# Performance work log

Measured on AMD Instinct MI355X. Metric: run time of the kernel, lower is better.

The kernel has to match this reference:

```python
import jax, jax.numpy as jnp
import numpy as np

N_NODES = 50000
DEG = 16
N_EDGES = N_NODES * DEG  # 800000
C_IN = 64
C_OUT = 64


def setup_inputs() -> dict:
    key = jax.random.key(0)
    k_x, k_src, k_ea, k_w, k_b = jax.random.split(key, 5)
    x = jax.random.normal(k_x, (N_NODES, C_IN), dtype=jnp.float32)
    # Every node appears DEG times as a destination -> no empty segments in max-aggregation.
    dst = jnp.repeat(jnp.arange(N_NODES, dtype=jnp.int32), DEG)
    src = jax.random.randint(k_src, (N_EDGES,), 0, N_NODES, dtype=jnp.int32)
    edge_index = jnp.stack([src, dst], axis=0)  # [2, E], row0=source(j), row1=target(i)
    edge_attr = jax.random.normal(k_ea, (N_EDGES, 1), dtype=jnp.float32)  # unused by forward (faithful to source)
    # MLP(2*C_IN -> C_OUT): Linear weight [out, 2*in] + bias, kaiming-ish scale
    W = jax.random.normal(k_w, (C_OUT, 2 * C_IN), dtype=jnp.float32) * (1.0 / np.sqrt(2 * C_IN))
    b = jax.random.normal(k_b, (C_OUT,), dtype=jnp.float32) * 0.01
    return {"x": x, "edge_index": edge_index, "edge_attr": edge_attr, "W": W, "b": b}


def reference(x, edge_index, edge_attr, W, b):
    # PyG EdgeConv: out_i = max_{j in N(i)} MLP(concat(x_i, x_j - x_i)); aggr='max'
    src = edge_index[0]  # j (source)
    dst = edge_index[1]  # i (target)
    x_i = x[dst]                      # [E, C]
    x_j = x[src]                      # [E, C]
    feat = jnp.concatenate([x_i, x_j - x_i], axis=-1)   # [E, 2C]
    msg = jax.nn.relu(feat @ W.T + b)                    # [E, C_out] per-edge MLP
    out = jax.ops.segment_max(msg, dst, num_segments=x.shape[0])  # scatter-max
    # Guard against -inf for isolated nodes (none by construction, but match scatter fill=0)
    return jnp.where(jnp.isneginf(out), 0.0, out)
```

## Files before the change

### kernel.cpp

```cpp
#include <hip/hip_runtime.h>


#define DEG 16
#define C 64
#define NPW 16
#define WPB 4

typedef __attribute__((ext_vector_type(8))) short s16x8;
typedef __attribute__((ext_vector_type(4))) float f32x4;

__device__ __forceinline__ unsigned short f2bf(float f) {
    union { float f; unsigned u; } v; v.f = f;
    unsigned u = v.u + 0x7FFFu + ((v.u >> 16) & 1u);
    return (unsigned short)(u >> 16);
}

__global__ __launch_bounds__(256) void cvt_bf16(const float* __restrict__ x,
                                                unsigned short* __restrict__ xb,
                                                int n4) {
    int i = blockIdx.x * blockDim.x + threadIdx.x;
    if (i >= n4) return;
    f32x4 v = ((const f32x4*)x)[i];
    ushort4 o;
    o.x = f2bf(v[0]); o.y = f2bf(v[1]); o.z = f2bf(v[2]); o.w = f2bf(v[3]);
    ((ushort4*)xb)[i] = o;
}

template<bool PRE>
__device__ __forceinline__ s16x8 load_frag(const float* __restrict__ x,
                                           const unsigned short* __restrict__ xb,
                                           int row, int koff) {
    if constexpr (PRE) {
        return *(const s16x8*)(xb + row * C + koff);
    } else {
        const float* p = x + row * C + koff;
        f32x4 a = *(const f32x4*)p;
        f32x4 b = *(const f32x4*)(p + 4);
        s16x8 r;
        r[0] = (short)f2bf(a[0]); r[1] = (short)f2bf(a[1]);
        r[2] = (short)f2bf(a[2]); r[3] = (short)f2bf(a[3]);
        r[4] = (short)f2bf(b[0]); r[5] = (short)f2bf(b[1]);
        r[6] = (short)f2bf(b[2]); r[7] = (short)f2bf(b[3]);
        return r;
    }
}

template<bool PRE>
__global__ __launch_bounds__(256, 2) void edgeconv_mfma(
    const float* __restrict__ x,
    const unsigned short* __restrict__ xb,
    const int* __restrict__ src,
    const float* __restrict__ W,
    const float* __restrict__ bias,
    float* __restrict__ out,
    int n_groups)
{
    const int lane = threadIdx.x & 63;
    const int wave = threadIdx.x >> 6;
    const int col  = lane & 15;
    const int quad = lane >> 4;
    int group = blockIdx.x * WPB + wave;
    if (group >= n_groups) group = n_groups - 1;

    s16x8 b2[4][2];
    f32x4 baseD[4];
    {
        s16x8 bd[4][2];
        #pragma unroll
        for (int nt = 0; nt < 4; ++nt) {
            const float* wrow = W + (nt * 16 + col) * (2 * C);
            #pragma unroll
            for (int ks = 0; ks < 2; ++ks) {
                const int k0 = ks * 32 + quad * 8;
                f32x4 w1a = *(const f32x4*)(wrow + k0);
                f32x4 w1b = *(const f32x4*)(wrow + k0 + 4);
                f32x4 w2a = *(const f32x4*)(wrow + C + k0);
                f32x4 w2b = *(const f32x4*)(wrow + C + k0 + 4);
                s16x8 t2, td;
                #pragma unroll
                for (int j = 0; j < 4; ++j) {
                    t2[j]     = (short)f2bf(w2a[j]);
                    t2[j + 4] = (short)f2bf(w2b[j]);
                    td[j]     = (short)f2bf(w1a[j] - w2a[j]);
                    td[j + 4] = (short)f2bf(w1b[j] - w2b[j]);
                }
                b2[nt][ks] = t2;
                bd[nt][ks] = td;
            }
        }
        #pragma unroll
        for (int nt = 0; nt < 4; ++nt) {
            float bv = bias[nt * 16 + col];
            baseD[nt] = (f32x4){bv, bv, bv, bv};
        }
        const int nrow = group * NPW + col;
        s16x8 xi0 = load_frag<PRE>(x, xb, nrow, quad * 8);
        s16x8 xi1 = load_frag<PRE>(x, xb, nrow, 32 + quad * 8);
        #pragma unroll
        for (int nt = 0; nt < 4; ++nt) {
            baseD[nt] = __builtin_amdgcn_mfma_f32_16x16x32_bf16(xi0, bd[nt][0], baseD[nt], 0, 0, 0);
            baseD[nt] = __builtin_amdgcn_mfma_f32_16x16x32_bf16(xi1, bd[nt][1], baseD[nt], 0, 0, 0);
        }
    }

    int idx[NPW];
    #pragma unroll
    for (int n = 0; n < NPW; ++n)
        idx[n] = src[group * (NPW * DEG) + n * DEG + col];

    s16x8 xa[3][2];
    #pragma unroll
    for (int p = 0; p < 2; ++p) {
        xa[p][0] = load_frag<PRE>(x, xb, idx[p], quad * 8);
        xa[p][1] = load_frag<PRE>(x, xb, idx[p], 32 + quad * 8);
    }

    #pragma unroll
    for (int n = 0; n < NPW; ++n) {
        if (n + 2 < NPW) {
            xa[(n + 2) % 3][0] = load_frag<PRE>(x, xb, idx[n + 2], quad * 8);
            xa[(n + 2) % 3][1] = load_frag<PRE>(x, xb, idx[n + 2], 32 + quad * 8);
        }
        const int slane = ((n >> 2) << 4) | col;
        f32x4 acc[4];
        #pragma unroll
        for (int nt = 0; nt < 4; ++nt) {
            float bb = __shfl(baseD[nt][n & 3], slane);
            acc[nt] = (f32x4){bb, bb, bb, bb};
        }
        #pragma unroll
        for (int nt = 0; nt < 4; ++nt) {
            acc[nt] = __builtin_amdgcn_mfma_f32_16x16x32_bf16(xa[n % 3][0], b2[nt][0], acc[nt], 0, 0, 0);
            acc[nt] = __builtin_amdgcn_mfma_f32_16x16x32_bf16(xa[n % 3][1], b2[nt][1], acc[nt], 0, 0, 0);
        }
        float m[4];
        #pragma unroll
        for (int nt = 0; nt < 4; ++nt) {
            float t = fmaxf(fmaxf(acc[nt][0], acc[nt][1]),
                            fmaxf(acc[nt][2], acc[nt][3]));
            t = fmaxf(t, __shfl_xor(t, 16));
            t = fmaxf(t, __shfl_xor(t, 32));
            m[nt] = t;
        }
        float r = quad == 0 ? m[0] : quad == 1 ? m[1] : quad == 2 ? m[2] : m[3];
        r = fmaxf(r, 0.0f);
        out[(group * NPW + n) * C + lane] = r;
    }
}

extern "C" void kernel_launch(void* const* d_in, const int* in_sizes, int n_in,
                              void* d_out, int out_size, void* d_ws, size_t ws_size,
                              hipStream_t stream) {
    const float* x    = (const float*)d_in[0];
    const int*   src  = (const int*)  d_in[1];
    const float* W    = (const float*)d_in[3];
    const float* b    = (const float*)d_in[4];
    float*       out  = (float*)d_out;

    const int n_nodes  = in_sizes[0] / C;
    const int n_groups = (n_nodes + NPW - 1) / NPW;
    const int grid     = (n_groups + WPB - 1) / WPB;

    const size_t need = (size_t)n_nodes * C * sizeof(unsigned short);
    if (ws_size >= need) {
        unsigned short* xbuf = (unsigned short*)d_ws;
        const int n4 = n_nodes * C / 4;
        cvt_bf16<<<(n4 + 255) / 256, 256, 0, stream>>>(x, xbuf, n4);
        edgeconv_mfma<true><<<grid, 256, 0, stream>>>(x, xbuf, src, W, b, out, n_groups);
    } else {
        edgeconv_mfma<false><<<grid, 256, 0, stream>>>(x, nullptr, src, W, b, out, n_groups);
    }
}
```

Baseline: 109.7 us.

## Precompute bf16 weight fragments once and shrink per-wave node group to four

```diff
diff --git a/kernel.cpp b/kernel.cpp
--- a/kernel.cpp
+++ b/kernel.cpp
@@ -3,7 +3,7 @@
 
 #define DEG 16
 #define C 64
-#define NPW 16
+#define NPW 4
 #define WPB 4
 
 typedef __attribute__((ext_vector_type(8))) short s16x8;
@@ -15,57 +15,21 @@
     return (unsigned short)(u >> 16);
 }
 
-__global__ __launch_bounds__(256) void cvt_bf16(const float* __restrict__ x,
-                                                unsigned short* __restrict__ xb,
-                                                int n4) {
+
+__global__ __launch_bounds__(256) void prep(const float* __restrict__ x,
+                                            const float* __restrict__ W,
+                                            unsigned short* __restrict__ ws_u,
+                                            int n4) {
     int i = blockIdx.x * blockDim.x + threadIdx.x;
-    if (i >= n4) return;
-    f32x4 v = ((const f32x4*)x)[i];
-    ushort4 o;
-    o.x = f2bf(v[0]); o.y = f2bf(v[1]); o.z = f2bf(v[2]); o.w = f2bf(v[3]);
-    ((ushort4*)xb)[i] = o;
-}
-
-template<bool PRE>
-__device__ __forceinline__ s16x8 load_frag(const float* __restrict__ x,
-                                           const unsigned short* __restrict__ xb,
-                                           int row, int koff) {
-    if constexpr (PRE) {
-        return *(const s16x8*)(xb + row * C + koff);
-    } else {
-        const float* p = x + row * C + koff;
-        f32x4 a = *(const f32x4*)p;
-        f32x4 b = *(const f32x4*)(p + 4);
-        s16x8 r;
-        r[0] = (short)f2bf(a[0]); r[1] = (short)f2bf(a[1]);
-        r[2] = (short)f2bf(a[2]); r[3] = (short)f2bf(a[3]);
-        r[4] = (short)f2bf(b[0]); r[5] = (short)f2bf(b[1]);
-        r[6] = (short)f2bf(b[2]); r[7] = (short)f2bf(b[3]);
-        return r;
-    }
-}
-
-template<bool PRE>
-__global__ __launch_bounds__(256, 2) void edgeconv_mfma(
-    const float* __restrict__ x,
-    const unsigned short* __restrict__ xb,
-    const int* __restrict__ src,
-    const float* __restrict__ W,
-    const float* __restrict__ bias,
-    float* __restrict__ out,
-    int n_groups)
-{
-    const int lane = threadIdx.x & 63;
-    const int wave = threadIdx.x >> 6;
-    const int col  = lane & 15;
-    const int quad = lane >> 4;
-    int group = blockIdx.x * WPB + wave;
-    if (group >= n_groups) group = n_groups - 1;
-
-    s16x8 b2[4][2];
-    f32x4 baseD[4];
-    {
-        s16x8 bd[4][2];
+    if (i < n4) {
+        f32x4 v = ((const f32x4*)x)[i];
+        ushort4 o;
+        o.x = f2bf(v[0]); o.y = f2bf(v[1]); o.z = f2bf(v[2]); o.w = f2bf(v[3]);
+        ((ushort4*)ws_u)[i] = o;
+    }
+    if (blockIdx.x == 0 && threadIdx.x < 64) {
+        const int lane = threadIdx.x, col = lane & 15, quad = lane >> 4;
+        unsigned short* wf = ws_u + (size_t)n4 * 4;
         #pragma unroll
         for (int nt = 0; nt < 4; ++nt) {
             const float* wrow = W + (nt * 16 + col) * (2 * C);
@@ -84,54 +48,77 @@
                     td[j]     = (short)f2bf(w1a[j] - w2a[j]);
                     td[j + 4] = (short)f2bf(w1b[j] - w2b[j]);
                 }
-                b2[nt][ks] = t2;
-                bd[nt][ks] = td;
+                *(s16x8*)(wf + (((0 * 8) + nt * 2 + ks) * 64 + lane) * 8) = td;
+                *(s16x8*)(wf + (((1 * 8) + nt * 2 + ks) * 64 + lane) * 8) = t2;
             }
         }
-        #pragma unroll
-        for (int nt = 0; nt < 4; ++nt) {
-            float bv = bias[nt * 16 + col];
-            baseD[nt] = (f32x4){bv, bv, bv, bv};
-        }
-        const int nrow = group * NPW + col;
-        s16x8 xi0 = load_frag<PRE>(x, xb, nrow, quad * 8);
-        s16x8 xi1 = load_frag<PRE>(x, xb, nrow, 32 + quad * 8);
-        #pragma unroll
-        for (int nt = 0; nt < 4; ++nt) {
-            baseD[nt] = __builtin_amdgcn_mfma_f32_16x16x32_bf16(xi0, bd[nt][0], baseD[nt], 0, 0, 0);
-            baseD[nt] = __builtin_amdgcn_mfma_f32_16x16x32_bf16(xi1, bd[nt][1], baseD[nt], 0, 0, 0);
-        }
-    }
+    }
+}
+
+__global__ __launch_bounds__(256, 4) void edgeconv_mfma(
+    const unsigned short* __restrict__ xb,
+    const int* __restrict__ src,
+    const float* __restrict__ bias,
+    float* __restrict__ out,
+    int n_groups, int n_nodes)
+{
+    const int lane = threadIdx.x & 63;
+    const int wave = threadIdx.x >> 6;
+    const int col  = lane & 15;
+    const int quad = lane >> 4;
+    int group = blockIdx.x * WPB + wave;
+    if (group >= n_groups) group = n_groups - 1;
+    const int node0 = group * NPW;
 
     int idx[NPW];
     #pragma unroll
     for (int n = 0; n < NPW; ++n)
-        idx[n] = src[group * (NPW * DEG) + n * DEG + col];
-
-    s16x8 xa[3][2];
-    #pragma unroll
-    for (int p = 0; p < 2; ++p) {
-        xa[p][0] = load_frag<PRE>(x, xb, idx[p], quad * 8);
-        xa[p][1] = load_frag<PRE>(x, xb, idx[p], 32 + quad * 8);
-    }
-
+        idx[n] = src[node0 * DEG + n * DEG + col];
+
+    const unsigned short* wf = xb + (size_t)n_nodes * C;
+    s16x8 bd[4][2], b2[4][2];
+    #pragma unroll
+    for (int nt = 0; nt < 4; ++nt)
+        #pragma unroll
+        for (int ks = 0; ks < 2; ++ks) {
+            bd[nt][ks] = *(const s16x8*)(wf + ((nt * 2 + ks) * 64 + lane) * 8);
+            b2[nt][ks] = *(const s16x8*)(wf + ((8 + nt * 2 + ks) * 64 + lane) * 8);
+        }
+
+    const int xirow = node0 + (col & 3);
+    s16x8 xi0 = *(const s16x8*)(xb + xirow * C + quad * 8);
+    s16x8 xi1 = *(const s16x8*)(xb + xirow * C + 32 + quad * 8);
+    f32x4 baseD[4];
+    #pragma unroll
+    for (int nt = 0; nt < 4; ++nt) {
+        float bv = bias[nt * 16 + col];
+        baseD[nt] = (f32x4){bv, bv, bv, bv};
+    }
+    #pragma unroll
+    for (int nt = 0; nt < 4; ++nt) {
+        baseD[nt] = __builtin_amdgcn_mfma_f32_16x16x32_bf16(xi0, bd[nt][0], baseD[nt], 0, 0, 0);
+        baseD[nt] = __builtin_amdgcn_mfma_f32_16x16x32_bf16(xi1, bd[nt][1], baseD[nt], 0, 0, 0);
+    }
+
+    s16x8 xa[NPW][2];
     #pragma unroll
     for (int n = 0; n < NPW; ++n) {
-        if (n + 2 < NPW) {
-            xa[(n + 2) % 3][0] = load_frag<PRE>(x, xb, idx[n + 2], quad * 8);
-            xa[(n + 2) % 3][1] = load_frag<PRE>(x, xb, idx[n + 2], 32 + quad * 8);
-        }
-        const int slane = ((n >> 2) << 4) | col;
+        xa[n][0] = *(const s16x8*)(xb + idx[n] * C + quad * 8);
+        xa[n][1] = *(const s16x8*)(xb + idx[n] * C + 32 + quad * 8);
+    }
+
+    #pragma unroll
+    for (int n = 0; n < NPW; ++n) {
         f32x4 acc[4];
         #pragma unroll
         for (int nt = 0; nt < 4; ++nt) {
-            float bb = __shfl(baseD[nt][n & 3], slane);
+            float bb = __shfl(baseD[nt][n], col);
             acc[nt] = (f32x4){bb, bb, bb, bb};
         }
         #pragma unroll
         for (int nt = 0; nt < 4; ++nt) {
-            acc[nt] = __builtin_amdgcn_mfma_f32_16x16x32_bf16(xa[n % 3][0], b2[nt][0], acc[nt], 0, 0, 0);
-            acc[nt] = __builtin_amdgcn_mfma_f32_16x16x32_bf16(xa[n % 3][1], b2[nt][1], acc[nt], 0, 0, 0);
+            acc[nt] = __builtin_amdgcn_mfma_f32_16x16x32_bf16(xa[n][0], b2[nt][0], acc[nt], 0, 0, 0);
+            acc[nt] = __builtin_amdgcn_mfma_f32_16x16x32_bf16(xa[n][1], b2[nt][1], acc[nt], 0, 0, 0);
         }
         float m[4];
         #pragma unroll
@@ -144,7 +131,105 @@
         }
         float r = quad == 0 ? m[0] : quad == 1 ? m[1] : quad == 2 ? m[2] : m[3];
         r = fmaxf(r, 0.0f);
-        out[(group * NPW + n) * C + lane] = r;
+        out[(node0 + n) * C + lane] = r;
+    }
+}
+
+__global__ __launch_bounds__(256, 2) void edgeconv_fallback(
+    const float* __restrict__ x, const int* __restrict__ src,
+    const float* __restrict__ W, const float* __restrict__ bias,
+    float* __restrict__ out, int n_groups)
+{
+    const int lane = threadIdx.x & 63, wave = threadIdx.x >> 6;
+    const int col = lane & 15, quad = lane >> 4;
+    int group = blockIdx.x * WPB + wave;
+    if (group >= n_groups) group = n_groups - 1;
+
+    auto frag = [&](int row, int koff) {
+        const float* p = x + row * C + koff;
+        f32x4 a = *(const f32x4*)p, b = *(const f32x4*)(p + 4);
+        s16x8 r;
+        #pragma unroll
+        for (int j = 0; j < 4; ++j) {
+            r[j] = (short)f2bf(a[j]); r[j + 4] = (short)f2bf(b[j]);
+        }
+        return r;
+    };
+
+    s16x8 b2[4][2];
+    f32x4 baseD[4];
+    {
+        s16x8 bd[4][2];
+        #pragma unroll
+        for (int nt = 0; nt < 4; ++nt) {
+            const float* wrow = W + (nt * 16 + col) * (2 * C);
+            #pragma unroll
+            for (int ks = 0; ks < 2; ++ks) {
+                const int k0 = ks * 32 + quad * 8;
+                f32x4 w1a = *(const f32x4*)(wrow + k0);
+                f32x4 w1b = *(const f32x4*)(wrow + k0 + 4);
+                f32x4 w2a = *(const f32x4*)(wrow + C + k0);
+                f32x4 w2b = *(const f32x4*)(wrow + C + k0 + 4);
+                s16x8 t2, td;
+                #pragma unroll
+                for (int j = 0; j < 4; ++j) {
+                    t2[j] = (short)f2bf(w2a[j]); t2[j + 4] = (short)f2bf(w2b[j]);
+                    td[j] = (short)f2bf(w1a[j] - w2a[j]);
+                    td[j + 4] = (short)f2bf(w1b[j] - w2b[j]);
+                }
+                b2[nt][ks] = t2; bd[nt][ks] = td;
+            }
+        }
+        #pragma unroll
+        for (int nt = 0; nt < 4; ++nt) {
+            float bv = bias[nt * 16 + col];
+            baseD[nt] = (f32x4){bv, bv, bv, bv};
+        }
+        const int nrow = group * 16 + col;
+        s16x8 xi0 = frag(nrow, quad * 8), xi1 = frag(nrow, 32 + quad * 8);
+        #pragma unroll
+        for (int nt = 0; nt < 4; ++nt) {
+            baseD[nt] = __builtin_amdgcn_mfma_f32_16x16x32_bf16(xi0, bd[nt][0], baseD[nt], 0, 0, 0);
+            baseD[nt] = __builtin_amdgcn_mfma_f32_16x16x32_bf16(xi1, bd[nt][1], baseD[nt], 0, 0, 0);
+        }
+    }
+    int idx[16];
+    #pragma unroll
+    for (int n = 0; n < 16; ++n) idx[n] = src[group * 256 + n * DEG + col];
+    s16x8 xa[3][2];
+    #pragma unroll
+    for (int p = 0; p < 2; ++p) {
+        xa[p][0] = frag(idx[p], quad * 8); xa[p][1] = frag(idx[p], 32 + quad * 8);
+    }
+    #pragma unroll
+    for (int n = 0; n < 16; ++n) {
+        if (n + 2 < 16) {
+            xa[(n + 2) % 3][0] = frag(idx[n + 2], quad * 8);
+            xa[(n + 2) % 3][1] = frag(idx[n + 2], 32 + quad * 8);
+        }
+        const int slane = ((n >> 2) << 4) | col;
+        f32x4 acc[4];
+        #pragma unroll
+        for (int nt = 0; nt < 4; ++nt) {
+            float bb = __shfl(baseD[nt][n & 3], slane);
+            acc[nt] = (f32x4){bb, bb, bb, bb};
+        }
+        #pragma unroll
+        for (int nt = 0; nt < 4; ++nt) {
+            acc[nt] = __builtin_amdgcn_mfma_f32_16x16x32_bf16(xa[n % 3][0], b2[nt][0], acc[nt], 0, 0, 0);
+            acc[nt] = __builtin_amdgcn_mfma_f32_16x16x32_bf16(xa[n % 3][1], b2[nt][1], acc[nt], 0, 0, 0);
+        }
+        float m[4];
+        #pragma unroll
+        for (int nt = 0; nt < 4; ++nt) {
+            float t = fmaxf(fmaxf(acc[nt][0], acc[nt][1]),
+                            fmaxf(acc[nt][2], acc[nt][3]));
+            t = fmaxf(t, __shfl_xor(t, 16));
+            t = fmaxf(t, __shfl_xor(t, 32));
+            m[nt] = t;
+        }
+        float r = quad == 0 ? m[0] : quad == 1 ? m[1] : quad == 2 ? m[2] : m[3];
+        out[(group * 16 + n) * C + lane] = fmaxf(r, 0.0f);
     }
 }
 
@@ -157,17 +242,19 @@
     const float* b    = (const float*)d_in[4];
     float*       out  = (float*)d_out;
 
-    const int n_nodes  = in_sizes[0] / C;
-    const int n_groups = (n_nodes + NPW - 1) / NPW;
-    const int grid     = (n_groups + WPB - 1) / WPB;
-
-    const size_t need = (size_t)n_nodes * C * sizeof(unsigned short);
+    const int n_nodes = in_sizes[0] / C;
+    const size_t need = ((size_t)n_nodes * C + 16 * 64 * 8) * sizeof(unsigned short);
+
     if (ws_size >= need) {
-        unsigned short* xbuf = (unsigned short*)d_ws;
+        unsigned short* ws_u = (unsigned short*)d_ws;
         const int n4 = n_nodes * C / 4;
-        cvt_bf16<<<(n4 + 255) / 256, 256, 0, stream>>>(x, xbuf, n4);
-        edgeconv_mfma<true><<<grid, 256, 0, stream>>>(x, xbuf, src, W, b, out, n_groups);
+        const int n_groups = (n_nodes + NPW - 1) / NPW;
+        const int grid = (n_groups + WPB - 1) / WPB;
+        prep<<<(n4 + 255) / 256, 256, 0, stream>>>(x, W, ws_u, n4);
+        edgeconv_mfma<<<grid, 256, 0, stream>>>(ws_u, src, b, out, n_groups, n_nodes);
     } else {
-        edgeconv_mfma<false><<<grid, 256, 0, stream>>>(x, nullptr, src, W, b, out, n_groups);
-    }
-}
+        const int n_groups = (n_nodes + 15) / 16;
+        edgeconv_fallback<<<(n_groups + WPB - 1) / WPB, 256, 0, stream>>>(
+            x, src, W, b, out, n_groups);
+    }
+}
```

Result: faster. 100.1 us (-8.8%).

## Fuse bf16 conversion into gather, halve nodes per wave, deepen prefetch

Applied to the files above, without the earlier changes.

```diff
diff --git a/kernel.cpp b/kernel.cpp
--- a/kernel.cpp
+++ b/kernel.cpp
@@ -1,58 +1,44 @@
 #include <hip/hip_runtime.h>
+#include <hip/hip_bf16.h>
 
 
 #define DEG 16
 #define C 64
-#define NPW 16
+#define NPW 8
 #define WPB 4
+#define PIPE 4
 
 typedef __attribute__((ext_vector_type(8))) short s16x8;
 typedef __attribute__((ext_vector_type(4))) float f32x4;
 
-__device__ __forceinline__ unsigned short f2bf(float f) {
-    union { float f; unsigned u; } v; v.f = f;
-    unsigned u = v.u + 0x7FFFu + ((v.u >> 16) & 1u);
-    return (unsigned short)(u >> 16);
+__device__ __forceinline__ unsigned pk2(float lo, float hi) {
+    __hip_bfloat162 h = __float22bfloat162_rn(make_float2(lo, hi));
+    union { __hip_bfloat162 h; unsigned u; } c; c.h = h;
+    return c.u;
 }
 
-__global__ __launch_bounds__(256) void cvt_bf16(const float* __restrict__ x,
-                                                unsigned short* __restrict__ xb,
-                                                int n4) {
-    int i = blockIdx.x * blockDim.x + threadIdx.x;
-    if (i >= n4) return;
-    f32x4 v = ((const f32x4*)x)[i];
-    ushort4 o;
-    o.x = f2bf(v[0]); o.y = f2bf(v[1]); o.z = f2bf(v[2]); o.w = f2bf(v[3]);
-    ((ushort4*)xb)[i] = o;
+__device__ __forceinline__ s16x8 cvt_frag(f32x4 a, f32x4 b) {
+    union { unsigned u[4]; s16x8 v; } r;
+    r.u[0] = pk2(a[0], a[1]); r.u[1] = pk2(a[2], a[3]);
+    r.u[2] = pk2(b[0], b[1]); r.u[3] = pk2(b[2], b[3]);
+    return r.v;
 }
 
-template<bool PRE>
-__device__ __forceinline__ s16x8 load_frag(const float* __restrict__ x,
-                                           const unsigned short* __restrict__ xb,
-                                           int row, int koff) {
-    if constexpr (PRE) {
-        return *(const s16x8*)(xb + row * C + koff);
-    } else {
-        const float* p = x + row * C + koff;
-        f32x4 a = *(const f32x4*)p;
-        f32x4 b = *(const f32x4*)(p + 4);
-        s16x8 r;
-        r[0] = (short)f2bf(a[0]); r[1] = (short)f2bf(a[1]);
-        r[2] = (short)f2bf(a[2]); r[3] = (short)f2bf(a[3]);
-        r[4] = (short)f2bf(b[0]); r[5] = (short)f2bf(b[1]);
-        r[6] = (short)f2bf(b[2]); r[7] = (short)f2bf(b[3]);
-        return r;
-    }
+__device__ __forceinline__ void load4(f32x4* d, const float* __restrict__ x,
+                                      int row, int quad) {
+    const float* p = x + row * C + quad * 8;
+    d[0] = *(const f32x4*)p;
+    d[1] = *(const f32x4*)(p + 4);
+    d[2] = *(const f32x4*)(p + 32);
+    d[3] = *(const f32x4*)(p + 36);
 }
 
-template<bool PRE>
-__global__ __launch_bounds__(256, 2) void edgeconv_mfma(
+__global__ __launch_bounds__(256, 3) void edgeconv_fused(
     const float* __restrict__ x,
-    const unsigned short* __restrict__ xb,
-    const int* __restrict__ src,
+    const int*   __restrict__ src,
     const float* __restrict__ W,
     const float* __restrict__ bias,
-    float* __restrict__ out,
+    float*       __restrict__ out,
     int n_groups)
 {
     const int lane = threadIdx.x & 63;
@@ -61,66 +47,60 @@
     const int quad = lane >> 4;
     int group = blockIdx.x * WPB + wave;
     if (group >= n_groups) group = n_groups - 1;
-
-    s16x8 b2[4][2];
-    f32x4 baseD[4];
-    {
-        s16x8 bd[4][2];
-        #pragma unroll
-        for (int nt = 0; nt < 4; ++nt) {
-            const float* wrow = W + (nt * 16 + col) * (2 * C);
-            #pragma unroll
-            for (int ks = 0; ks < 2; ++ks) {
-                const int k0 = ks * 32 + quad * 8;
-                f32x4 w1a = *(const f32x4*)(wrow + k0);
-                f32x4 w1b = *(const f32x4*)(wrow + k0 + 4);
-                f32x4 w2a = *(const f32x4*)(wrow + C + k0);
-                f32x4 w2b = *(const f32x4*)(wrow + C + k0 + 4);
-                s16x8 t2, td;
-                #pragma unroll
-                for (int j = 0; j < 4; ++j) {
-                    t2[j]     = (short)f2bf(w2a[j]);
-                    t2[j + 4] = (short)f2bf(w2b[j]);
-                    td[j]     = (short)f2bf(w1a[j] - w2a[j]);
-                    td[j + 4] = (short)f2bf(w1b[j] - w2b[j]);
-                }
-                b2[nt][ks] = t2;
-                bd[nt][ks] = td;
-            }
-        }
-        #pragma unroll
-        for (int nt = 0; nt < 4; ++nt) {
-            float bv = bias[nt * 16 + col];
-            baseD[nt] = (f32x4){bv, bv, bv, bv};
-        }
-        const int nrow = group * NPW + col;
-        s16x8 xi0 = load_frag<PRE>(x, xb, nrow, quad * 8);
-        s16x8 xi1 = load_frag<PRE>(x, xb, nrow, 32 + quad * 8);
-        #pragma unroll
-        for (int nt = 0; nt < 4; ++nt) {
-            baseD[nt] = __builtin_amdgcn_mfma_f32_16x16x32_bf16(xi0, bd[nt][0], baseD[nt], 0, 0, 0);
-            baseD[nt] = __builtin_amdgcn_mfma_f32_16x16x32_bf16(xi1, bd[nt][1], baseD[nt], 0, 0, 0);
-        }
-    }
+    const int node0 = group * NPW;
 
     int idx[NPW];
     #pragma unroll
     for (int n = 0; n < NPW; ++n)
-        idx[n] = src[group * (NPW * DEG) + n * DEG + col];
+        idx[n] = src[node0 * DEG + n * DEG + col];
 
-    s16x8 xa[3][2];
+    f32x4 xf[PIPE][4];
     #pragma unroll
-    for (int p = 0; p < 2; ++p) {
-        xa[p][0] = load_frag<PRE>(x, xb, idx[p], quad * 8);
-        xa[p][1] = load_frag<PRE>(x, xb, idx[p], 32 + quad * 8);
+    for (int p = 0; p < PIPE; ++p)
+        load4(xf[p], x, idx[p], quad);
+
+    s16x8 bd[4][2], b2[4][2];
+    #pragma unroll
+    for (int nt = 0; nt < 4; ++nt) {
+        const float* wrow = W + (nt * 16 + col) * (2 * C);
+        #pragma unroll
+        for (int ks = 0; ks < 2; ++ks) {
+            const int k0 = ks * 32 + quad * 8;
+            f32x4 w1a = *(const f32x4*)(wrow + k0);
+            f32x4 w1b = *(const f32x4*)(wrow + k0 + 4);
+            f32x4 w2a = *(const f32x4*)(wrow + C + k0);
+            f32x4 w2b = *(const f32x4*)(wrow + C + k0 + 4);
+            b2[nt][ks] = cvt_frag(w2a, w2b);
+            f32x4 da, db;
+            #pragma unroll
+            for (int j = 0; j < 4; ++j) { da[j] = w1a[j] - w2a[j]; db[j] = w1b[j] - w2b[j]; }
+            bd[nt][ks] = cvt_frag(da, db);
+        }
+    }
+
+    f32x4 xif[4];
+    load4(xif, x, node0 + (col & 7), quad);
+    s16x8 xi0 = cvt_frag(xif[0], xif[1]);
+    s16x8 xi1 = cvt_frag(xif[2], xif[3]);
+    f32x4 baseD[4];
+    #pragma unroll
+    for (int nt = 0; nt < 4; ++nt) {
+        float bv = bias[nt * 16 + col];
+        baseD[nt] = (f32x4){bv, bv, bv, bv};
+    }
+    #pragma unroll
+    for (int nt = 0; nt < 4; ++nt) {
+        baseD[nt] = __builtin_amdgcn_mfma_f32_16x16x32_bf16(xi0, bd[nt][0], baseD[nt], 0, 0, 0);
+        baseD[nt] = __builtin_amdgcn_mfma_f32_16x16x32_bf16(xi1, bd[nt][1], baseD[nt], 0, 0, 0);
     }
 
     #pragma unroll
     for (int n = 0; n < NPW; ++n) {
-        if (n + 2 < NPW) {
-            xa[(n + 2) % 3][0] = load_frag<PRE>(x, xb, idx[n + 2], quad * 8);
-            xa[(n + 2) % 3][1] = load_frag<PRE>(x, xb, idx[n + 2], 32 + quad * 8);
-        }
+        s16x8 fa0 = cvt_frag(xf[n % PIPE][0], xf[n % PIPE][1]);
+        s16x8 fa1 = cvt_frag(xf[n % PIPE][2], xf[n % PIPE][3]);
+        if (n + PIPE < NPW)
+            load4(xf[n % PIPE], x, idx[n + PIPE], quad);
+
         const int slane = ((n >> 2) << 4) | col;
         f32x4 acc[4];
         #pragma unroll
@@ -130,8 +110,8 @@
         }
         #pragma unroll
         for (int nt = 0; nt < 4; ++nt) {
-            acc[nt] = __builtin_amdgcn_mfma_f32_16x16x32_bf16(xa[n % 3][0], b2[nt][0], acc[nt], 0, 0, 0);
-            acc[nt] = __builtin_amdgcn_mfma_f32_16x16x32_bf16(xa[n % 3][1], b2[nt][1], acc[nt], 0, 0, 0);
+            acc[nt] = __builtin_amdgcn_mfma_f32_16x16x32_bf16(fa0, b2[nt][0], acc[nt], 0, 0, 0);
+            acc[nt] = __builtin_amdgcn_mfma_f32_16x16x32_bf16(fa1, b2[nt][1], acc[nt], 0, 0, 0);
         }
         float m[4];
         #pragma unroll
@@ -144,7 +124,7 @@
         }
         float r = quad == 0 ? m[0] : quad == 1 ? m[1] : quad == 2 ? m[2] : m[3];
         r = fmaxf(r, 0.0f);
-        out[(group * NPW + n) * C + lane] = r;
+        out[(node0 + n) * C + lane] = r;
     }
 }
 
@@ -161,13 +141,5 @@
     const int n_groups = (n_nodes + NPW - 1) / NPW;
     const int grid     = (n_groups + WPB - 1) / WPB;
 
-    const size_t need = (size_t)n_nodes * C * sizeof(unsigned short);
-    if (ws_size >= need) {
-        unsigned short* xbuf = (unsigned short*)d_ws;
-        const int n4 = n_nodes * C / 4;
-        cvt_bf16<<<(n4 + 255) / 256, 256, 0, stream>>>(x, xbuf, n4);
-        edgeconv_mfma<true><<<grid, 256, 0, stream>>>(x, xbuf, src, W, b, out, n_groups);
-    } else {
-        edgeconv_mfma<false><<<grid, 256, 0, stream>>>(x, nullptr, src, W, b, out, n_groups);
-    }
+    edgeconv_fused<<<grid, 256, 0, stream>>>(x, src, W, b, out, n_groups);
 }
```

Result: slower. 126.9 us (+15.6%).
